# Optimization experiments

Measured on AMD Instinct MI355X. Metric: run time of the kernel, lower is better.

The kernel has to match this reference:

```python
import jax, jax.numpy as jnp
import numpy as np

N_POOL, DIM_EMB, DIM_HID, FIRST_DIM = 4, 128, 128, 134
N_NODES_TOT, N_GRAPHS = 250000, 256
EPS = 1e-16  # PyG softmax eps


def setup_inputs() -> dict:
    key = jax.random.key(0)
    ks = jax.random.split(key, 20)
    inp = {
        "x": jax.random.normal(ks[0], (N_NODES_TOT, FIRST_DIM), jnp.float32),
        "batch": jnp.sort(jax.random.randint(ks[1], (N_NODES_TOT,), 0, N_GRAPHS)),
        "n_nodes": jax.random.uniform(ks[2], (N_GRAPHS, 1), jnp.float32),
        "Omegas": jax.random.uniform(ks[3], (N_GRAPHS, 1), jnp.float32),
        "Phis": jax.random.uniform(ks[4], (N_GRAPHS, 1), jnp.float32),
        "Lambdas": jax.random.uniform(ks[5], (N_GRAPHS, 1), jnp.float32),
        "Omegas_norm": jax.random.uniform(ks[6], (N_GRAPHS, 1), jnp.float32),
        "Phis_norm": jax.random.uniform(ks[7], (N_GRAPHS, 1), jnp.float32),
        "Lambdas_norm": jax.random.uniform(ks[8], (N_GRAPHS, 1), jnp.float32),
    }
    s1 = 1.0 / np.sqrt(FIRST_DIM)
    s2 = 1.0 / np.sqrt(DIM_HID)
    # stacked params for the n_pool GlobalAttention modules
    inp["gate_w1"] = jax.random.uniform(ks[9], (N_POOL, FIRST_DIM, DIM_HID), jnp.float32, -s1, s1)
    inp["gate_b1"] = jax.random.uniform(ks[10], (N_POOL, DIM_HID), jnp.float32, -s1, s1)
    inp["gate_w2"] = jax.random.uniform(ks[11], (N_POOL, DIM_HID), jnp.float32, -s2, s2)
    inp["gate_b2"] = jax.random.uniform(ks[12], (N_POOL,), jnp.float32, -s2, s2)
    inp["nn_w1"] = jax.random.uniform(ks[13], (N_POOL, FIRST_DIM, DIM_HID), jnp.float32, -s1, s1)
    inp["nn_b1"] = jax.random.uniform(ks[14], (N_POOL, DIM_HID), jnp.float32, -s1, s1)
    inp["nn_w2"] = jax.random.uniform(ks[15], (N_POOL, DIM_HID, DIM_EMB), jnp.float32, -s2, s2)
    inp["nn_b2"] = jax.random.uniform(ks[16], (N_POOL, DIM_EMB), jnp.float32, -s2, s2)
    return inp


def reference(x, batch, n_nodes, Omegas, Phis, Lambdas, Omegas_norm, Phis_norm,
              Lambdas_norm, gate_w1, gate_b1, gate_w2, gate_b2, nn_w1, nn_b1,
              nn_w2, nn_b2):
    B = n_nodes.shape[0]
    # gate scores: per-node scalar per pool head -> [N, K]
    g1 = jax.nn.relu(jnp.einsum("nf,kfh->nkh", x, gate_w1) + gate_b1)
    scores = jnp.einsum("nkh,kh->nk", g1, gate_w2) + gate_b2
    # batch-segmented softmax (stable, PyG style)
    m = jax.ops.segment_max(scores, batch, num_segments=B)          # [B, K]
    e = jnp.exp(scores - m[batch])                                  # [N, K]
    denom = jax.ops.segment_sum(e, batch, num_segments=B)[batch] + EPS
    gate = e / denom                                                # [N, K]
    # node transform per pool -> [N, K, D]
    h1 = jax.nn.relu(jnp.einsum("nf,kfh->nkh", x, nn_w1) + nn_b1)
    v = jnp.einsum("nkh,khd->nkd", h1, nn_w2) + nn_b2
    # gated segment-sum pooling -> [B, K, D], concat pools -> [B, K*D]
    pooled = jax.ops.segment_sum(gate[..., None] * v, batch, num_segments=B)
    ctx_emb = pooled.reshape(B, N_POOL * DIM_EMB)
    return jnp.concatenate(
        [ctx_emb, n_nodes, Omegas, Phis, Lambdas, Omegas_norm, Phis_norm,
         Lambdas_norm], axis=1)
```

## Files before the change

### kernel.cpp

```cpp
#include <hip/hip_runtime.h>
#include <math.h>

#define N_NODES 250000
#define F_DIM   134
#define H_DIM   128
#define K_POOL  4
#define B_GR    256
#define EPSF    1e-16f
#define OUT_W   (K_POOL * H_DIM + 7)

#define BM      128
#define BK      32
#define KP      160
#define KSTEPS  5
#define GMAX    4
#define NBLK    ((N_NODES + BM - 1) / BM)
#define N_PAD   (NBLK * BM)

#define SZ_X       (N_PAD * KP * 2)
#define SZ_W       (K_POOL * H_DIM * KP * 2)
#define OFF_XH     0
#define OFF_XL     (OFF_XH + SZ_X)
#define OFF_WHG    (OFF_XL + SZ_X)
#define OFF_WLG    (OFF_WHG + SZ_W)
#define OFF_WHN    (OFF_WLG + SZ_W)
#define OFF_WLN    (OFF_WHN + SZ_W)
#define OFF_SCORES (OFF_WLN + SZ_W)
#define OFF_SEG    (OFF_SCORES + N_NODES * 16)
#define OFF_MAX    (OFF_SEG + 2048)
#define OFF_DEN    (OFF_MAX + 4096)
#define OFF_POOL   (OFF_DEN + 4096)

typedef __attribute__((ext_vector_type(8))) short bf16x8;
typedef __attribute__((ext_vector_type(4))) float f32x4;

__device__ __forceinline__ ushort f2bf(float f) {
    union { float f; unsigned u; } v; v.f = f;
    const unsigned u = v.u;
    return (ushort)((u + 0x7FFFu + ((u >> 16) & 1u)) >> 16);
}
__device__ __forceinline__ float bf2f(ushort h) {
    union { unsigned u; float f; } v; v.u = ((unsigned)h) << 16; return v.f;
}
__device__ __forceinline__ int swz(int row, int kg) {
    return ((row << 6) + (kg << 4)) ^ ((row & 7) << 4);
}

__launch_bounds__(256)
__global__ void cvt_x_kernel(const float* __restrict__ x,
                             ushort* __restrict__ xh, ushort* __restrict__ xl)
{
    const int idx = (blockIdx.x * 256 + threadIdx.x) * 4;
    if (idx >= N_PAD * KP) return;
    const int row = idx / KP;
    const int col = idx - row * KP;
    float v[4] = {0.f, 0.f, 0.f, 0.f};
    if (row < N_NODES) {
        const float* xr = x + row * F_DIM + col;
        if (col + 4 <= F_DIM) {
            float2 a = *(const float2*)(xr);
            float2 b = *(const float2*)(xr + 2);
            v[0] = a.x; v[1] = a.y; v[2] = b.x; v[3] = b.y;
        } else if (col < F_DIM) {
            float2 a = *(const float2*)(xr);
            v[0] = a.x; v[1] = a.y;
        }
    }
    ushort4 h, l;
    h.x = f2bf(v[0]); l.x = f2bf(v[0] - bf2f(h.x));
    h.y = f2bf(v[1]); l.y = f2bf(v[1] - bf2f(h.y));
    h.z = f2bf(v[2]); l.z = f2bf(v[2] - bf2f(h.z));
    h.w = f2bf(v[3]); l.w = f2bf(v[3] - bf2f(h.w));
    *(ushort4*)(xh + idx) = h;
    *(ushort4*)(xl + idx) = l;
}

__launch_bounds__(256)
__global__ void cvt_w_kernel(const float* __restrict__ wg, const float* __restrict__ wn,
                             ushort* __restrict__ whg, ushort* __restrict__ wlg,
                             ushort* __restrict__ whn, ushort* __restrict__ wln)
{
    const int idx = blockIdx.x * 256 + threadIdx.x;
    if (idx >= K_POOL * H_DIM * KP) return;
    const int k   = idx % KP;
    const int pc  = idx / KP;
    const int col = pc & 127, p = pc >> 7;
    const float* src = blockIdx.y ? wn : wg;
    const float v = (k < F_DIM) ? src[(p * F_DIM + k) * H_DIM + col] : 0.f;
    const ushort h = f2bf(v);
    const ushort lo = f2bf(v - bf2f(h));
    if (blockIdx.y) { whn[idx] = h; wln[idx] = lo; }
    else            { whg[idx] = h; wlg[idx] = lo; }
}

__device__ __forceinline__ void mm_stage(const ushort* __restrict__ Ahs,
                                         const ushort* __restrict__ Als,
                                         const ushort* __restrict__ Bhs,
                                         const ushort* __restrict__ Bls,
                                         int kbeg, int t,
                                         short* Ah, short* Al, short* Bh, short* Bl)
{
    const int row  = t >> 1;
    const int half = t & 1;
    const int base = row * KP + kbeg + half * 16;
    const int off0 = swz(row, half * 2) >> 1;
    const int off1 = swz(row, half * 2 + 1) >> 1;
    *(bf16x8*)(Ah + off0) = *(const bf16x8*)(Ahs + base);
    *(bf16x8*)(Ah + off1) = *(const bf16x8*)(Ahs + base + 8);
    *(bf16x8*)(Al + off0) = *(const bf16x8*)(Als + base);
    *(bf16x8*)(Al + off1) = *(const bf16x8*)(Als + base + 8);
    *(bf16x8*)(Bh + off0) = *(const bf16x8*)(Bhs + base);
    *(bf16x8*)(Bh + off1) = *(const bf16x8*)(Bhs + base + 8);
    *(bf16x8*)(Bl + off0) = *(const bf16x8*)(Bls + base);
    *(bf16x8*)(Bl + off1) = *(const bf16x8*)(Bls + base + 8);
}

__device__ __forceinline__ void mm_compute(int t, const short* Ah, const short* Al,
                                           const short* Bh, const short* Bl,
                                           f32x4 acc[2][8])
{
    const int lane = t & 63, wv = t >> 6;
    bf16x8 ah[2], al[2];
#pragma unroll
    for (int r = 0; r < 2; ++r) {
        const int rowA = wv * 32 + r * 16 + (lane & 15);
        const int off  = swz(rowA, lane >> 4) >> 1;
        ah[r] = *(const bf16x8*)(Ah + off);
        al[r] = *(const bf16x8*)(Al + off);
    }
#pragma unroll
    for (int c = 0; c < 8; ++c) {
        const int rowB = c * 16 + (lane & 15);
        const int off  = swz(rowB, lane >> 4) >> 1;
        const bf16x8 bh = *(const bf16x8*)(Bh + off);
        const bf16x8 bl = *(const bf16x8*)(Bl + off);
#pragma unroll
        for (int r = 0; r < 2; ++r) {
            acc[r][c] = __builtin_amdgcn_mfma_f32_16x16x32_bf16(ah[r], bh, acc[r][c], 0, 0, 0);
            acc[r][c] = __builtin_amdgcn_mfma_f32_16x16x32_bf16(ah[r], bl, acc[r][c], 0, 0, 0);
            acc[r][c] = __builtin_amdgcn_mfma_f32_16x16x32_bf16(al[r], bh, acc[r][c], 0, 0, 0);
        }
    }
}

__global__ void seg_kernel(const int* __restrict__ batch, int* __restrict__ seg) {
    int b = blockIdx.x * blockDim.x + threadIdx.x;
    if (b > B_GR) return;
    int lo = 0, hi = N_NODES;
    while (lo < hi) {
        int mid = (lo + hi) >> 1;
        if (batch[mid] < b) lo = mid + 1; else hi = mid;
    }
    seg[b] = lo;
}

__launch_bounds__(256, 2)
__global__ void gate_kernel(const ushort* __restrict__ xh, const ushort* __restrict__ xl,
                            const ushort* __restrict__ wh, const ushort* __restrict__ wl,
                            const float* __restrict__ b1,
                            const float* __restrict__ w2,
                            const float* __restrict__ b2,
                            float* __restrict__ scores)
{
    __shared__ short Ah[4096], Al[4096], Bh[4096], Bl[4096];
    const int m0 = blockIdx.x * BM, t = threadIdx.x;
    const int lane = t & 63, wv = t >> 6;
    const ushort* Ahs = xh + (long)m0 * KP;
    const ushort* Als = xl + (long)m0 * KP;

    for (int k = 0; k < K_POOL; ++k) {
        const ushort* Bhs = wh + k * H_DIM * KP;
        const ushort* Bls = wl + k * H_DIM * KP;

        f32x4 acc[2][8];
        const f32x4 z = {0.f, 0.f, 0.f, 0.f};
#pragma unroll
        for (int r = 0; r < 2; ++r)
#pragma unroll
            for (int c = 0; c < 8; ++c) acc[r][c] = z;

        for (int ks = 0; ks < KSTEPS; ++ks) {
            __syncthreads();
            mm_stage(Ahs, Als, Bhs, Bls, ks * BK, t, Ah, Al, Bh, Bl);
            __syncthreads();
            mm_compute(t, Ah, Al, Bh, Bl, acc);
        }

        float b1v[8], w2v[8];
#pragma unroll
        for (int c = 0; c < 8; ++c) {
            const int col = c * 16 + (lane & 15);
            b1v[c] = b1[k * H_DIM + col];
            w2v[c] = w2[k * H_DIM + col];
        }
        const float b2v = b2[k];
#pragma unroll
        for (int r = 0; r < 2; ++r)
#pragma unroll
            for (int q = 0; q < 4; ++q) {
                float s = 0.f;
#pragma unroll
                for (int c = 0; c < 8; ++c)
                    s = fmaf(fmaxf(acc[r][c][q] + b1v[c], 0.f), w2v[c], s);
                s += __shfl_xor(s, 1); s += __shfl_xor(s, 2);
                s += __shfl_xor(s, 4); s += __shfl_xor(s, 8);
                if ((lane & 15) == 0) {
                    const int m = m0 + wv * 32 + r * 16 + (lane >> 4) * 4 + q;
                    if (m < N_NODES) scores[m * 4 + k] = s + b2v;
                }
            }
    }
}

__launch_bounds__(256)
__global__ void stats_kernel(const float* __restrict__ scores,
                             const int* __restrict__ seg,
                             float* __restrict__ maxv,
                             float* __restrict__ denom,
                             float* __restrict__ pooled)
{
    const int g = blockIdx.x;
    const int t = threadIdx.x;
    const int s = seg[g], e = seg[g + 1];
    const float4* sc4 = (const float4*)scores;

    float mx[4] = {-INFINITY, -INFINITY, -INFINITY, -INFINITY};
    for (int n = s + t; n < e; n += 256) {
        float4 v = sc4[n];
        mx[0] = fmaxf(mx[0], v.x); mx[1] = fmaxf(mx[1], v.y);
        mx[2] = fmaxf(mx[2], v.z); mx[3] = fmaxf(mx[3], v.w);
    }
#pragma unroll
    for (int c = 0; c < 4; ++c)
        for (int off = 32; off; off >>= 1)
            mx[c] = fmaxf(mx[c], __shfl_down(mx[c], off));

    __shared__ float redbuf[4][4];
    __shared__ float bmax[4];
    const int wid = t >> 6, lane = t & 63;
    if (lane == 0)
#pragma unroll
        for (int c = 0; c < 4; ++c) redbuf[wid][c] = mx[c];
    __syncthreads();
    if (t == 0)
#pragma unroll
        for (int c = 0; c < 4; ++c) {
            float m = redbuf[0][c];
            m = fmaxf(m, redbuf[1][c]); m = fmaxf(m, redbuf[2][c]); m = fmaxf(m, redbuf[3][c]);
            bmax[c] = m;
        }
    __syncthreads();
    const float m0v = bmax[0], m1v = bmax[1], m2v = bmax[2], m3v = bmax[3];

    float sm[4] = {0.f, 0.f, 0.f, 0.f};
    for (int n = s + t; n < e; n += 256) {
        float4 v = sc4[n];
        sm[0] += expf(v.x - m0v); sm[1] += expf(v.y - m1v);
        sm[2] += expf(v.z - m2v); sm[3] += expf(v.w - m3v);
    }
#pragma unroll
    for (int c = 0; c < 4; ++c)
        for (int off = 32; off; off >>= 1)
            sm[c] += __shfl_down(sm[c], off);
    __syncthreads();
    if (lane == 0)
#pragma unroll
        for (int c = 0; c < 4; ++c) redbuf[wid][c] = sm[c];
    __syncthreads();
    if (t == 0)
#pragma unroll
        for (int c = 0; c < 4; ++c) {
            maxv[g * 4 + c]  = bmax[c];
            denom[g * 4 + c] = redbuf[0][c] + redbuf[1][c] + redbuf[2][c] + redbuf[3][c] + EPSF;
        }
    pooled[g * 512 + t]       = 0.f;
    pooled[g * 512 + 256 + t] = 0.f;
}

__launch_bounds__(256, 2)
__global__ void pool_kernel(const ushort* __restrict__ xh, const ushort* __restrict__ xl,
                            const ushort* __restrict__ wh, const ushort* __restrict__ wl,
                            const int* __restrict__ batch,
                            const float* __restrict__ b1,
                            const float* __restrict__ scores,
                            const float* __restrict__ maxv,
                            const float* __restrict__ denom,
                            float* __restrict__ pooled)
{
    __shared__ short Ah[4096], Al[4096], Bh[4096], Bl[4096];
    __shared__ float lds_pool[GMAX][K_POOL][H_DIM];
    const int m0 = blockIdx.x * BM, t = threadIdx.x;
    const int lane = t & 63, wv = t >> 6;
    const ushort* Ahs = xh + (long)m0 * KP;
    const ushort* Als = xl + (long)m0 * KP;

    for (int idx = t; idx < GMAX * K_POOL * H_DIM; idx += 256)
        ((float*)lds_pool)[idx] = 0.f;

    const int gfirst0 = batch[m0];

    for (int k = 0; k < K_POOL; ++k) {
        const ushort* Bhs = wh + k * H_DIM * KP;
        const ushort* Bls = wl + k * H_DIM * KP;

        f32x4 acc[2][8];
        const f32x4 z = {0.f, 0.f, 0.f, 0.f};
#pragma unroll
        for (int r = 0; r < 2; ++r)
#pragma unroll
            for (int c = 0; c < 8; ++c) acc[r][c] = z;

        for (int ks = 0; ks < KSTEPS; ++ks) {
            __syncthreads();
            mm_stage(Ahs, Als, Bhs, Bls, ks * BK, t, Ah, Al, Bh, Bl);
            __syncthreads();
            mm_compute(t, Ah, Al, Bh, Bl, acc);
        }

        float b1v[8];
#pragma unroll
        for (int c = 0; c < 8; ++c)
            b1v[c] = b1[k * H_DIM + c * 16 + (lane & 15)];

#pragma unroll
        for (int r = 0; r < 2; ++r) {
            const int mrow = m0 + wv * 32 + r * 16;
            if (mrow >= N_NODES) continue;
            const int mhi   = (mrow + 15 < N_NODES) ? mrow + 15 : N_NODES - 1;
            const int ga    = batch[mrow];
            const bool unif = (batch[mhi] == ga) && (mrow + 15 < N_NODES);
            if (unif) {
                const float mxv = maxv[ga * 4 + k];
                const float den = denom[ga * 4 + k];
                float gates[4];
#pragma unroll
                for (int q = 0; q < 4; ++q) {
                    const int m = mrow + (lane >> 4) * 4 + q;
                    gates[q] = expf(scores[m * 4 + k] - mxv) / den;
                }
                const int lg = ga - gfirst0;
#pragma unroll
                for (int c = 0; c < 8; ++c) {
                    float p = 0.f;
#pragma unroll
                    for (int q = 0; q < 4; ++q)
                        p = fmaf(gates[q], fmaxf(acc[r][c][q] + b1v[c], 0.f), p);
                    p += __shfl_xor(p, 16);
                    p += __shfl_xor(p, 32);
                    if (lane < 16) {
                        if (lg < GMAX) atomicAdd(&lds_pool[lg][k][c * 16 + lane], p);
                        else atomicAdd(&pooled[(ga * K_POOL + k) * H_DIM + c * 16 + lane], p);
                    }
                }
            } else {
#pragma unroll
                for (int q = 0; q < 4; ++q) {
                    const int m = mrow + (lane >> 4) * 4 + q;
                    const bool val = m < N_NODES;
                    int g = ga; float gate = 0.f;
                    if (val) {
                        g = batch[m];
                        gate = expf(scores[m * 4 + k] - maxv[g * 4 + k]) / denom[g * 4 + k];
                    }
                    const int lg = g - gfirst0;
#pragma unroll
                    for (int c = 0; c < 8; ++c) {
                        const float v = gate * fmaxf(acc[r][c][q] + b1v[c], 0.f);
                        if (val && v != 0.f) {
                            if (lg < GMAX) atomicAdd(&lds_pool[lg][k][c * 16 + (lane & 15)], v);
                            else atomicAdd(&pooled[(g * K_POOL + k) * H_DIM + c * 16 + (lane & 15)], v);
                        }
                    }
                }
            }
        }
    }

    __syncthreads();
    {
        const int mlast = (m0 + BM - 1 < N_NODES) ? m0 + BM - 1 : N_NODES - 1;
        int span = batch[mlast] - gfirst0 + 1;
        if (span > GMAX) span = GMAX;
        for (int idx = t; idx < span * K_POOL * H_DIM; idx += 256) {
            const float v = ((const float*)lds_pool)[idx];
            if (v != 0.f) {
                const int lg  = idx >> 9;
                const int rem = idx & 511;
                atomicAdd(&pooled[(gfirst0 + lg) * 512 + rem], v);
            }
        }
    }
}

__launch_bounds__(128)
__global__ void out_kernel(const float* __restrict__ pooled,
                           const float* __restrict__ w2,
                           const float* __restrict__ b2,
                           const float* __restrict__ denom,
                           const float* __restrict__ s0, const float* __restrict__ s1,
                           const float* __restrict__ s2, const float* __restrict__ s3,
                           const float* __restrict__ s4, const float* __restrict__ s5,
                           const float* __restrict__ s6,
                           float* __restrict__ out)
{
    const int g = blockIdx.x;
    const int t = threadIdx.x;
    __shared__ float ps[H_DIM];
    float* orow = out + g * OUT_W;

    for (int k = 0; k < K_POOL; ++k) {
        __syncthreads();
        ps[t] = pooled[(g * K_POOL + k) * H_DIM + t];
        __syncthreads();
        const float den = denom[g * 4 + k];
        const float gs  = (den - EPSF) / den;
        float a = b2[k * H_DIM + t] * gs;
        const float* wkt = w2 + (k * H_DIM) * H_DIM + t;
#pragma unroll 4
        for (int h = 0; h < H_DIM; ++h)
            a = fmaf(ps[h], wkt[h * H_DIM], a);
        orow[k * H_DIM + t] = a;
    }
    if (t < 7) {
        const float* sp;
        switch (t) {
            case 0: sp = s0; break; case 1: sp = s1; break; case 2: sp = s2; break;
            case 3: sp = s3; break; case 4: sp = s4; break; case 5: sp = s5; break;
            default: sp = s6; break;
        }
        orow[K_POOL * H_DIM + t] = sp[g];
    }
}

extern "C" void kernel_launch(void* const* d_in, const int* in_sizes, int n_in,
                              void* d_out, int out_size, void* d_ws, size_t ws_size,
                              hipStream_t stream) {
    const float* x     = (const float*)d_in[0];
    const int*   batch = (const int*)d_in[1];
    const float* n_nodes = (const float*)d_in[2];
    const float* Omegas  = (const float*)d_in[3];
    const float* Phis    = (const float*)d_in[4];
    const float* Lambdas = (const float*)d_in[5];
    const float* Omn     = (const float*)d_in[6];
    const float* Phn     = (const float*)d_in[7];
    const float* Lan     = (const float*)d_in[8];
    const float* gw1 = (const float*)d_in[9];
    const float* gb1 = (const float*)d_in[10];
    const float* gw2 = (const float*)d_in[11];
    const float* gb2 = (const float*)d_in[12];
    const float* nw1 = (const float*)d_in[13];
    const float* nb1 = (const float*)d_in[14];
    const float* nw2 = (const float*)d_in[15];
    const float* nb2 = (const float*)d_in[16];

    char* ws = (char*)d_ws;
    ushort* xh  = (ushort*)(ws + OFF_XH);
    ushort* xl  = (ushort*)(ws + OFF_XL);
    ushort* whg = (ushort*)(ws + OFF_WHG);
    ushort* wlg = (ushort*)(ws + OFF_WLG);
    ushort* whn = (ushort*)(ws + OFF_WHN);
    ushort* wln = (ushort*)(ws + OFF_WLN);
    float* scores = (float*)(ws + OFF_SCORES);
    int*   seg    = (int*)(ws + OFF_SEG);
    float* maxv   = (float*)(ws + OFF_MAX);
    float* denom  = (float*)(ws + OFF_DEN);
    float* pooled = (float*)(ws + OFF_POOL);
    float* out    = (float*)d_out;

    cvt_x_kernel<<<(N_PAD * KP / 4 + 255) / 256, 256, 0, stream>>>(x, xh, xl);
    dim3 wgrid((K_POOL * H_DIM * KP + 255) / 256, 2);
    cvt_w_kernel<<<wgrid, 256, 0, stream>>>(gw1, nw1, whg, wlg, whn, wln);
    seg_kernel<<<2, 256, 0, stream>>>(batch, seg);

    gate_kernel<<<NBLK, 256, 0, stream>>>(xh, xl, whg, wlg, gb1, gw2, gb2, scores);
    stats_kernel<<<B_GR, 256, 0, stream>>>(scores, seg, maxv, denom, pooled);
    pool_kernel<<<NBLK, 256, 0, stream>>>(xh, xl, whn, wln, batch, nb1,
                                          scores, maxv, denom, pooled);
    out_kernel<<<B_GR, 128, 0, stream>>>(pooled, nw2, nb2, denom,
                                         n_nodes, Omegas, Phis, Lambdas, Omn, Phn, Lan, out);
}
```

Measured before the change: 707.3 us.

## Pre-tile and pre-swizzle bf16 operands, stage via global_load_lds direct copies

```diff
diff --git a/kernel.cpp b/kernel.cpp
--- a/kernel.cpp
+++ b/kernel.cpp
@@ -11,21 +11,20 @@
 
 #define BM      128
 #define BK      32
-#define KP      160
 #define KSTEPS  5
 #define GMAX    4
 #define NBLK    ((N_NODES + BM - 1) / BM)
-#define N_PAD   (NBLK * BM)
-
-#define SZ_X       (N_PAD * KP * 2)
-#define SZ_W       (K_POOL * H_DIM * KP * 2)
+#define TILE_USH 4096
+
+#define SZ_XT      (NBLK * KSTEPS * TILE_USH * 2)
+#define SZ_WT      (K_POOL * KSTEPS * TILE_USH * 2)
 #define OFF_XH     0
-#define OFF_XL     (OFF_XH + SZ_X)
-#define OFF_WHG    (OFF_XL + SZ_X)
-#define OFF_WLG    (OFF_WHG + SZ_W)
-#define OFF_WHN    (OFF_WLG + SZ_W)
-#define OFF_WLN    (OFF_WHN + SZ_W)
-#define OFF_SCORES (OFF_WLN + SZ_W)
+#define OFF_XL     (OFF_XH + SZ_XT)
+#define OFF_WHG    (OFF_XL + SZ_XT)
+#define OFF_WLG    (OFF_WHG + SZ_WT)
+#define OFF_WHN    (OFF_WLG + SZ_WT)
+#define OFF_WLN    (OFF_WHN + SZ_WT)
+#define OFF_SCORES (OFF_WLN + SZ_WT)
 #define OFF_SEG    (OFF_SCORES + N_NODES * 16)
 #define OFF_MAX    (OFF_SEG + 2048)
 #define OFF_DEN    (OFF_MAX + 4096)
@@ -46,33 +45,54 @@
     return ((row << 6) + (kg << 4)) ^ ((row & 7) << 4);
 }
 
+__device__ __forceinline__ void gld16(const ushort* g, ushort* l) {
+    __builtin_amdgcn_global_load_lds(
+        (const __attribute__((address_space(1))) unsigned*)g,
+        (__attribute__((address_space(3))) unsigned*)l, 16, 0, 0);
+}
+
 __launch_bounds__(256)
 __global__ void cvt_x_kernel(const float* __restrict__ x,
                              ushort* __restrict__ xh, ushort* __restrict__ xl)
 {
-    const int idx = (blockIdx.x * 256 + threadIdx.x) * 4;
-    if (idx >= N_PAD * KP) return;
-    const int row = idx / KP;
-    const int col = idx - row * KP;
-    float v[4] = {0.f, 0.f, 0.f, 0.f};
-    if (row < N_NODES) {
-        const float* xr = x + row * F_DIM + col;
-        if (col + 4 <= F_DIM) {
-            float2 a = *(const float2*)(xr);
-            float2 b = *(const float2*)(xr + 2);
-            v[0] = a.x; v[1] = a.y; v[2] = b.x; v[3] = b.y;
-        } else if (col < F_DIM) {
-            float2 a = *(const float2*)(xr);
-            v[0] = a.x; v[1] = a.y;
-        }
-    }
-    ushort4 h, l;
-    h.x = f2bf(v[0]); l.x = f2bf(v[0] - bf2f(h.x));
-    h.y = f2bf(v[1]); l.y = f2bf(v[1] - bf2f(h.y));
-    h.z = f2bf(v[2]); l.z = f2bf(v[2] - bf2f(h.z));
-    h.w = f2bf(v[3]); l.w = f2bf(v[3] - bf2f(h.w));
-    *(ushort4*)(xh + idx) = h;
-    *(ushort4*)(xl + idx) = l;
+    const int u = blockIdx.x * 256 + threadIdx.x;
+    if (u >= NBLK * KSTEPS * 512) return;
+    const int tile = u >> 9;
+    const int e    = u & 511;
+    const int row  = e >> 2, kg = e & 3;
+    const int blk  = tile / KSTEPS, ks = tile - blk * KSTEPS;
+    const int node = blk * BM + row;
+    const int col0 = ks * BK + kg * 8;
+
+    float v[8];
+#pragma unroll
+    for (int j = 0; j < 8; ++j) v[j] = 0.f;
+    if (node < N_NODES) {
+        const float* xr = x + (long)node * F_DIM + col0;
+        if (col0 + 8 <= F_DIM) {
+#pragma unroll
+            for (int j = 0; j < 4; ++j) {
+                float2 a = *(const float2*)(xr + 2 * j);
+                v[2 * j] = a.x; v[2 * j + 1] = a.y;
+            }
+        } else if (col0 < F_DIM) {
+#pragma unroll
+            for (int j = 0; j < 3; ++j) {
+                float2 a = *(const float2*)(xr + 2 * j);
+                v[2 * j] = a.x; v[2 * j + 1] = a.y;
+            }
+        }
+    }
+    bf16x8 h, l;
+#pragma unroll
+    for (int j = 0; j < 8; ++j) {
+        const ushort hh = f2bf(v[j]);
+        h[j] = (short)hh;
+        l[j] = (short)f2bf(v[j] - bf2f(hh));
+    }
+    const long dst = (long)tile * TILE_USH + (swz(row, kg) >> 1);
+    *(bf16x8*)(xh + dst) = h;
+    *(bf16x8*)(xl + dst) = l;
 }
 
 __launch_bounds__(256)
@@ -80,43 +100,53 @@
                              ushort* __restrict__ whg, ushort* __restrict__ wlg,
                              ushort* __restrict__ whn, ushort* __restrict__ wln)
 {
-    const int idx = blockIdx.x * 256 + threadIdx.x;
-    if (idx >= K_POOL * H_DIM * KP) return;
-    const int k   = idx % KP;
-    const int pc  = idx / KP;
-    const int col = pc & 127, p = pc >> 7;
+    const int u = blockIdx.x * 256 + threadIdx.x;
+    if (u >= K_POOL * KSTEPS * 512) return;
+    const int tile = u >> 9;
+    const int e    = u & 511;
+    const int col  = e >> 2, kg = e & 3;
+    const int head = tile / KSTEPS, ks = tile - head * KSTEPS;
+    const int k0   = ks * BK + kg * 8;
     const float* src = blockIdx.y ? wn : wg;
-    const float v = (k < F_DIM) ? src[(p * F_DIM + k) * H_DIM + col] : 0.f;
-    const ushort h = f2bf(v);
-    const ushort lo = f2bf(v - bf2f(h));
-    if (blockIdx.y) { whn[idx] = h; wln[idx] = lo; }
-    else            { whg[idx] = h; wlg[idx] = lo; }
-}
-
-__device__ __forceinline__ void mm_stage(const ushort* __restrict__ Ahs,
-                                         const ushort* __restrict__ Als,
-                                         const ushort* __restrict__ Bhs,
-                                         const ushort* __restrict__ Bls,
-                                         int kbeg, int t,
-                                         short* Ah, short* Al, short* Bh, short* Bl)
-{
-    const int row  = t >> 1;
-    const int half = t & 1;
-    const int base = row * KP + kbeg + half * 16;
-    const int off0 = swz(row, half * 2) >> 1;
-    const int off1 = swz(row, half * 2 + 1) >> 1;
-    *(bf16x8*)(Ah + off0) = *(const bf16x8*)(Ahs + base);
-    *(bf16x8*)(Ah + off1) = *(const bf16x8*)(Ahs + base + 8);
-    *(bf16x8*)(Al + off0) = *(const bf16x8*)(Als + base);
-    *(bf16x8*)(Al + off1) = *(const bf16x8*)(Als + base + 8);
-    *(bf16x8*)(Bh + off0) = *(const bf16x8*)(Bhs + base);
-    *(bf16x8*)(Bh + off1) = *(const bf16x8*)(Bhs + base + 8);
-    *(bf16x8*)(Bl + off0) = *(const bf16x8*)(Bls + base);
-    *(bf16x8*)(Bl + off1) = *(const bf16x8*)(Bls + base + 8);
-}
-
-__device__ __forceinline__ void mm_compute(int t, const short* Ah, const short* Al,
-                                           const short* Bh, const short* Bl,
+    const float* sp  = src + ((long)head * F_DIM) * H_DIM + col;
+
+    float v[8];
+#pragma unroll
+    for (int j = 0; j < 8; ++j)
+        v[j] = (k0 + j < F_DIM) ? sp[(k0 + j) * H_DIM] : 0.f;
+    bf16x8 h, l;
+#pragma unroll
+    for (int j = 0; j < 8; ++j) {
+        const ushort hh = f2bf(v[j]);
+        h[j] = (short)hh;
+        l[j] = (short)f2bf(v[j] - bf2f(hh));
+    }
+    const long dst = (long)tile * TILE_USH + (swz(col, kg) >> 1);
+    if (blockIdx.y) { *(bf16x8*)(whn + dst) = h; *(bf16x8*)(wln + dst) = l; }
+    else            { *(bf16x8*)(whg + dst) = h; *(bf16x8*)(wlg + dst) = l; }
+}
+
+__device__ __forceinline__ void stage_ks(const ushort* __restrict__ Ath,
+                                         const ushort* __restrict__ Atl,
+                                         const ushort* __restrict__ Bth,
+                                         const ushort* __restrict__ Btl,
+                                         ushort* lds, int t)
+{
+    const int wv  = t >> 6;
+    const int wo  = wv * 1024;
+    const int lo8 = (t & 63) * 8;
+    gld16(Ath + wo + lo8,       lds + wo);
+    gld16(Ath + wo + 512 + lo8, lds + wo + 512);
+    gld16(Atl + wo + lo8,       lds + 4096 + wo);
+    gld16(Atl + wo + 512 + lo8, lds + 4096 + wo + 512);
+    gld16(Bth + wo + lo8,       lds + 8192 + wo);
+    gld16(Bth + wo + 512 + lo8, lds + 8192 + wo + 512);
+    gld16(Btl + wo + lo8,       lds + 12288 + wo);
+    gld16(Btl + wo + 512 + lo8, lds + 12288 + wo + 512);
+}
+
+__device__ __forceinline__ void mm_compute(int t, const ushort* Ah, const ushort* Al,
+                                           const ushort* Bh, const ushort* Bl,
                                            f32x4 acc[2][8])
 {
     const int lane = t & 63, wv = t >> 6;
@@ -162,15 +192,15 @@
                             const float* __restrict__ b2,
                             float* __restrict__ scores)
 {
-    __shared__ short Ah[4096], Al[4096], Bh[4096], Bl[4096];
+    __shared__ ushort slds[16384];
     const int m0 = blockIdx.x * BM, t = threadIdx.x;
     const int lane = t & 63, wv = t >> 6;
-    const ushort* Ahs = xh + (long)m0 * KP;
-    const ushort* Als = xl + (long)m0 * KP;
+    const ushort* Ath = xh + (long)blockIdx.x * KSTEPS * TILE_USH;
+    const ushort* Atl = xl + (long)blockIdx.x * KSTEPS * TILE_USH;
 
     for (int k = 0; k < K_POOL; ++k) {
-        const ushort* Bhs = wh + k * H_DIM * KP;
-        const ushort* Bls = wl + k * H_DIM * KP;
+        const ushort* Bth = wh + (long)k * KSTEPS * TILE_USH;
+        const ushort* Btl = wl + (long)k * KSTEPS * TILE_USH;
 
         f32x4 acc[2][8];
         const f32x4 z = {0.f, 0.f, 0.f, 0.f};
@@ -181,9 +211,10 @@
 
         for (int ks = 0; ks < KSTEPS; ++ks) {
             __syncthreads();
-            mm_stage(Ahs, Als, Bhs, Bls, ks * BK, t, Ah, Al, Bh, Bl);
+            stage_ks(Ath + ks * TILE_USH, Atl + ks * TILE_USH,
+                     Bth + ks * TILE_USH, Btl + ks * TILE_USH, slds, t);
             __syncthreads();
-            mm_compute(t, Ah, Al, Bh, Bl, acc);
+            mm_compute(t, slds, slds + 4096, slds + 8192, slds + 12288, acc);
         }
 
         float b1v[8], w2v[8];
@@ -287,12 +318,12 @@
                             const float* __restrict__ denom,
                             float* __restrict__ pooled)
 {
-    __shared__ short Ah[4096], Al[4096], Bh[4096], Bl[4096];
+    __shared__ ushort slds[16384];
     __shared__ float lds_pool[GMAX][K_POOL][H_DIM];
     const int m0 = blockIdx.x * BM, t = threadIdx.x;
     const int lane = t & 63, wv = t >> 6;
-    const ushort* Ahs = xh + (long)m0 * KP;
-    const ushort* Als = xl + (long)m0 * KP;
+    const ushort* Ath = xh + (long)blockIdx.x * KSTEPS * TILE_USH;
+    const ushort* Atl = xl + (long)blockIdx.x * KSTEPS * TILE_USH;
 
     for (int idx = t; idx < GMAX * K_POOL * H_DIM; idx += 256)
         ((float*)lds_pool)[idx] = 0.f;
@@ -300,8 +331,8 @@
     const int gfirst0 = batch[m0];
 
     for (int k = 0; k < K_POOL; ++k) {
-        const ushort* Bhs = wh + k * H_DIM * KP;
-        const ushort* Bls = wl + k * H_DIM * KP;
+        const ushort* Bth = wh + (long)k * KSTEPS * TILE_USH;
+        const ushort* Btl = wl + (long)k * KSTEPS * TILE_USH;
 
         f32x4 acc[2][8];
         const f32x4 z = {0.f, 0.f, 0.f, 0.f};
@@ -312,9 +343,10 @@
 
         for (int ks = 0; ks < KSTEPS; ++ks) {
             __syncthreads();
-            mm_stage(Ahs, Als, Bhs, Bls, ks * BK, t, Ah, Al, Bh, Bl);
+            stage_ks(Ath + ks * TILE_USH, Atl + ks * TILE_USH,
+                     Bth + ks * TILE_USH, Btl + ks * TILE_USH, slds, t);
             __syncthreads();
-            mm_compute(t, Ah, Al, Bh, Bl, acc);
+            mm_compute(t, slds, slds + 4096, slds + 8192, slds + 12288, acc);
         }
 
         float b1v[8];
@@ -467,8 +499,8 @@
     float* pooled = (float*)(ws + OFF_POOL);
     float* out    = (float*)d_out;
 
-    cvt_x_kernel<<<(N_PAD * KP / 4 + 255) / 256, 256, 0, stream>>>(x, xh, xl);
-    dim3 wgrid((K_POOL * H_DIM * KP + 255) / 256, 2);
+    cvt_x_kernel<<<(NBLK * KSTEPS * 512) / 256, 256, 0, stream>>>(x, xh, xl);
+    dim3 wgrid((K_POOL * KSTEPS * 512 + 255) / 256, 2);
     cvt_w_kernel<<<wgrid, 256, 0, stream>>>(gw1, nw1, whg, wlg, whn, wln);
     seg_kernel<<<2, 256, 0, stream>>>(batch, seg);
 
```

Measured after the change: 623.7 us. 11.8% less time.
